# Optimization experiments

Hardware: AMD Instinct MI355X
Metric: run time of the kernel (lower is better)

Reference implementation:

```python
import jax, jax.numpy as jnp
import numpy as np

D_MODEL = 1024
NUM_HEADS = 16
D_HEAD = D_MODEL // NUM_HEADS


def setup_inputs() -> dict:
    key = jax.random.key(0)
    ks = jax.random.split(key, 7)
    B, S = 2, 2048
    scale = 1.0 / np.sqrt(D_MODEL)
    return {
        "x": jax.random.normal(ks[0], (B, S, D_MODEL), dtype=jnp.float32),
        "attn_weights": jnp.zeros((1,), dtype=jnp.float32),  # unused in original forward
        "Wq": jax.random.normal(ks[1], (D_MODEL, D_MODEL), dtype=jnp.float32) * scale,
        "Wk": jax.random.normal(ks[2], (D_MODEL, D_MODEL), dtype=jnp.float32) * scale,
        "Wv": jax.random.normal(ks[3], (D_MODEL, D_MODEL), dtype=jnp.float32) * scale,
        "Wp": jax.random.normal(ks[4], (D_MODEL, D_MODEL), dtype=jnp.float32) * scale,
        "bp": jnp.zeros((D_MODEL,), dtype=jnp.float32),
    }


def reference(x, attn_weights, Wq, Wk, Wv, Wp, bp):
    B, S, D = x.shape
    H, Dh = NUM_HEADS, D_HEAD
    # torch Linear: y = x @ W.T  (weights stored [out, in])
    q = (x @ Wq.T).reshape(B, S, H, Dh).transpose(0, 2, 1, 3)  # [B,H,S,Dh]
    k = (x @ Wk.T).reshape(B, S, H, Dh).transpose(0, 2, 1, 3)
    v = (x @ Wv.T).reshape(B, S, H, Dh).transpose(0, 2, 1, 3)
    # NOTE: original module applies NO 1/sqrt(d) scaling
    scores = jnp.einsum("bhqd,bhkd->bhqk", q, k)
    weights = jax.nn.softmax(scores, axis=-1)  # dropout is inference no-op
    out = jnp.einsum("bhqk,bhkd->bhqd", weights, v)
    out = out.transpose(0, 2, 1, 3).reshape(B, S, D)
    return out @ Wp.T + bp
```

## Files before the change

### kernel.cpp

```cpp
#include <hip/hip_runtime.h>
#include <hip/hip_bf16.h>

#define D_MODEL 1024
#define NUM_HEADS 16
#define D_HEAD 64
#define BATCH 2
#define SEQ 2048
#define TOKENS (BATCH * SEQ)

typedef __attribute__((ext_vector_type(8))) short bf16x8;
typedef __attribute__((ext_vector_type(4))) float f32x4;
typedef __attribute__((ext_vector_type(2))) unsigned int uint2v;

typedef __attribute__((address_space(1))) const unsigned int as1_uint;
typedef __attribute__((address_space(3))) unsigned int as3_uint;

#define LOG2E 1.44269504088896340736f

static __device__ __forceinline__ unsigned short f2bf(float f) {
    unsigned int u = __builtin_bit_cast(unsigned int, f);
    u += 0x7fffu + ((u >> 16) & 1u);
    return (unsigned short)(u >> 16);
}

static __device__ __forceinline__ unsigned int pk2bf(float a, float b) {
    __hip_bfloat162 h = __float22bfloat162_rn(float2{a, b});
    unsigned int u;
    __builtin_memcpy(&u, &h, 4);
    return u;
}

static __device__ __forceinline__ float fast_exp2(float x) {
    return __builtin_amdgcn_exp2f(x);
}

__global__ __launch_bounds__(256) void convert_bf16(
    const float* __restrict__ x,  const float* __restrict__ Wq,
    const float* __restrict__ Wk, const float* __restrict__ Wv,
    const float* __restrict__ Wp,
    unsigned short* __restrict__ xb,  unsigned short* __restrict__ Wqb,
    unsigned short* __restrict__ Wkb, unsigned short* __restrict__ Wvb,
    unsigned short* __restrict__ Wpb)
{
    int v = blockIdx.x * 256 + threadIdx.x;
    const float* s;
    unsigned short* d;
    int off;
    if (v < (1 << 20)) { s = x; d = xb; off = v; }
    else {
        int u = v - (1 << 20);
        int w = u >> 18;
        off = u & ((1 << 18) - 1);
        s = (w == 0) ? Wq : (w == 1) ? Wk : (w == 2) ? Wv : Wp;
        d = (w == 0) ? Wqb : (w == 1) ? Wkb : (w == 2) ? Wvb : Wpb;
    }
    float4 f = ((const float4*)s)[off];
    ushort4 o = { f2bf(f.x), f2bf(f.y), f2bf(f.z), f2bf(f.w) };
    ((ushort4*)d)[off] = o;
}

__global__ __launch_bounds__(512) void qkv_gemm(
    const unsigned short* __restrict__ xb,
    const unsigned short* __restrict__ Wqb, const unsigned short* __restrict__ Wkb,
    const unsigned short* __restrict__ Wvb,
    unsigned short* __restrict__ Q, unsigned short* __restrict__ Kb,
    unsigned short* __restrict__ Vt)
{
    const int m0 = blockIdx.x * 128;
    const int n0 = blockIdx.y * 128;
    const unsigned short* W = (blockIdx.z == 0) ? Wqb : (blockIdx.z == 1) ? Wkb : Wvb;

    __shared__ __attribute__((aligned(16))) unsigned short lA[128 * 64];
    __shared__ __attribute__((aligned(16))) unsigned short lB[128 * 64];

    const int t = threadIdx.x;
    const int wave = t >> 6, lane = t & 63;
    const int wm = (wave & 1) * 64, wn = (wave >> 1) * 32;
    const int l15 = lane & 15, quad = lane >> 4;
    const int sw = l15 & 7;

    f32x4 acc[4][2];
#pragma unroll
    for (int i = 0; i < 4; i++)
#pragma unroll
        for (int j = 0; j < 2; j++) acc[i][j] = (f32x4)0.f;

    for (int k0 = 0; k0 < D_MODEL; k0 += 64) {
        __syncthreads();
#pragma unroll
        for (int i = 0; i < 2; i++) {
            int fbase = wave * 64 + i * 512;
            int f = fbase + lane;
            int row = f >> 3, cp = f & 7;
            int c = cp ^ (row & 7);
            __builtin_amdgcn_global_load_lds(
                (as1_uint*)&xb[(size_t)(m0 + row) * D_MODEL + k0 + c * 8],
                (as3_uint*)&lA[fbase * 8], 16, 0, 0);
            __builtin_amdgcn_global_load_lds(
                (as1_uint*)&W[(size_t)(n0 + row) * D_MODEL + k0 + c * 8],
                (as3_uint*)&lB[fbase * 8], 16, 0, 0);
        }
        __syncthreads();

#pragma unroll
        for (int kk = 0; kk < 2; kk++) {
            const int cc = ((kk * 4 + quad) ^ sw) * 8;
            bf16x8 a[4], b[2];
#pragma unroll
            for (int mt = 0; mt < 4; mt++)
                a[mt] = *(const bf16x8*)&lA[(wm + mt * 16 + l15) * 64 + cc];
#pragma unroll
            for (int nt = 0; nt < 2; nt++)
                b[nt] = *(const bf16x8*)&lB[(wn + nt * 16 + l15) * 64 + cc];
#pragma unroll
            for (int mt = 0; mt < 4; mt++)
#pragma unroll
                for (int nt = 0; nt < 2; nt++)
                    acc[mt][nt] = __builtin_amdgcn_mfma_f32_16x16x32_bf16(
                        a[mt], b[nt], acc[mt][nt], 0, 0, 0);
        }
    }

    if (blockIdx.z == 2) {
        const int b = m0 >> 11;
        const int srow = (m0 & 2047) + wm + quad * 4;
#pragma unroll
        for (int mt = 0; mt < 4; mt++)
#pragma unroll
            for (int nt = 0; nt < 2; nt++) {
                int col = n0 + wn + nt * 16 + l15;
                int h = col >> 6, dh = col & 63;
                ushort4 pk = { f2bf(acc[mt][nt][0]), f2bf(acc[mt][nt][1]),
                               f2bf(acc[mt][nt][2]), f2bf(acc[mt][nt][3]) };
                *(ushort4*)&Vt[(size_t)((b * 16 + h) * 64 + dh) * SEQ + srow + mt * 16] = pk;
            }
    } else {
        unsigned short* Yo = (blockIdx.z == 0) ? Q : Kb;
        const float sc = (blockIdx.z == 0) ? LOG2E : 1.0f;
#pragma unroll
        for (int mt = 0; mt < 4; mt++)
#pragma unroll
            for (int nt = 0; nt < 2; nt++)
#pragma unroll
                for (int r = 0; r < 4; r++) {
                    int row = m0 + wm + mt * 16 + quad * 4 + r;
                    int col = n0 + wn + nt * 16 + l15;
                    Yo[(size_t)row * D_MODEL + col] = f2bf(acc[mt][nt][r] * sc);
                }
    }
}

__global__ __launch_bounds__(512, 4) void attn(
    const unsigned short* __restrict__ Q, const unsigned short* __restrict__ K,
    const unsigned short* __restrict__ Vt, unsigned short* __restrict__ O)
{
    const int q0 = blockIdx.x * 128;
    const int bh = blockIdx.y;
    const int b = bh >> 4, h = bh & 15;
    const size_t base = (size_t)b * SEQ * D_MODEL + (size_t)h * D_HEAD;
    const size_t baseV = (size_t)bh * D_HEAD * SEQ;

    __shared__ __attribute__((aligned(16))) char smem[40960];
    unsigned short* lK0 = (unsigned short*)&smem[0];
    unsigned short* lV0 = (unsigned short*)&smem[16384];

    const int t = threadIdx.x;
    const int wave = t >> 6, lane = t & 63;
    const int l15 = lane & 15, quad = lane >> 4;
    const int wq = wave & 3;
    const int sh = wave >> 2;
    const int qw = q0 + wq * 32;
    const int sbase = sh * (SEQ / 2);

    unsigned short* lK  = lK0 + sh * 4096;
    unsigned short* lVt = lV0 + sh * 4096;

    bf16x8 ones;
#pragma unroll
    for (int i = 0; i < 8; i++) ones[i] = (short)0x3F80;

    bf16x8 bq[2][2];
#pragma unroll
    for (int mq = 0; mq < 2; mq++)
#pragma unroll
        for (int kk = 0; kk < 2; kk++)
            bq[mq][kk] = *(const bf16x8*)&Q[base +
                (size_t)(qw + mq * 16 + l15) * D_MODEL + kk * 32 + quad * 8];

    const int tl = t & 255;
    const int r0 = tl >> 3, c0 = tl & 7;
    const int cs = (c0 ^ (r0 & 7)) * 8;
    const unsigned short* gK0 = &K[base + (size_t)(sbase + r0) * D_MODEL + c0 * 8];
    const unsigned short* gK1 = &K[base + (size_t)(sbase + r0 + 32) * D_MODEL + c0 * 8];
    const unsigned short* gV0 = &Vt[baseV + (size_t)r0 * SEQ + sbase + c0 * 8];
    const unsigned short* gV1 = &Vt[baseV + (size_t)(r0 + 32) * SEQ + sbase + c0 * 8];

    const int sw = l15 & 7;

    f32x4 o_acc[2][4];
#pragma unroll
    for (int i = 0; i < 2; i++)
#pragma unroll
        for (int j = 0; j < 4; j++) o_acc[i][j] = (f32x4)0.f;
    f32x4 o_l[2];
#pragma unroll
    for (int i = 0; i < 2; i++) o_l[i] = (f32x4)0.f;

    uint4 rK0 = *(const uint4*)gK0;
    uint4 rK1 = *(const uint4*)gK1;
    uint4 rV0 = *(const uint4*)gV0;
    uint4 rV1 = *(const uint4*)gV1;

    for (int s0 = 0; s0 < SEQ / 2; s0 += 64) {
        __syncthreads();
        *(uint4*)&lK[r0 * 64 + cs]        = rK0;
        *(uint4*)&lK[(r0 + 32) * 64 + cs] = rK1;
        *(uint4*)&lVt[r0 * 64 + cs]        = rV0;
        *(uint4*)&lVt[(r0 + 32) * 64 + cs] = rV1;
        __syncthreads();

        int sn = (s0 + 64 < SEQ / 2) ? s0 + 64 : 0;
        rK0 = *(const uint4*)(gK0 + (size_t)sn * D_MODEL);
        rK1 = *(const uint4*)(gK1 + (size_t)sn * D_MODEL);
        rV0 = *(const uint4*)(gV0 + sn);
        rV1 = *(const uint4*)(gV1 + sn);

        f32x4 st[4][2];
#pragma unroll
        for (int mt = 0; mt < 4; mt++)
#pragma unroll
            for (int mq = 0; mq < 2; mq++) st[mt][mq] = (f32x4)0.f;
#pragma unroll
        for (int kk = 0; kk < 2; kk++) {
            const int cc = ((kk * 4 + quad) ^ sw) * 8;
#pragma unroll
            for (int mt = 0; mt < 4; mt++) {
                bf16x8 ak = *(const bf16x8*)&lK[(mt * 16 + l15) * 64 + cc];
#pragma unroll
                for (int mq = 0; mq < 2; mq++)
                    st[mt][mq] = __builtin_amdgcn_mfma_f32_16x16x32_bf16(
                        ak, bq[mq][kk], st[mt][mq], 0, 0, 0);
            }
        }

#pragma unroll
        for (int mq = 0; mq < 2; mq++)
#pragma unroll
            for (int mt = 0; mt < 4; mt++)
#pragma unroll
                for (int r = 0; r < 4; r++)
                    st[mt][mq][r] = fast_exp2(st[mt][mq][r]);

        bf16x8 pa[2][2];
#pragma unroll
        for (int mq = 0; mq < 2; mq++)
#pragma unroll
            for (int kk = 0; kk < 2; kk++) {
                unsigned int cw[4];
#pragma unroll
                for (int j = 0; j < 2; j++) {
                    unsigned int w0 = pk2bf(st[2 * kk][mq][2 * j],
                                            st[2 * kk][mq][2 * j + 1]);
                    unsigned int w1 = pk2bf(st[2 * kk + 1][mq][2 * j],
                                            st[2 * kk + 1][mq][2 * j + 1]);
                    uint2v uv = __builtin_amdgcn_permlane32_swap(w0, w1, false, false);
                    uint2v f  = __builtin_amdgcn_permlane16_swap(uv[0], uv[1], false, false);
                    cw[j]     = f[0];
                    cw[2 + j] = f[1];
                }
                union { unsigned int w[4]; bf16x8 v; } u;
                u.w[0] = cw[0]; u.w[1] = cw[1]; u.w[2] = cw[2]; u.w[3] = cw[3];
                pa[mq][kk] = u.v;
            }

#pragma unroll
        for (int kk = 0; kk < 2; kk++) {
            const int cc = ((kk * 4 + quad) ^ sw) * 8;
            bf16x8 bv[4];
#pragma unroll
            for (int nt = 0; nt < 4; nt++)
                bv[nt] = *(const bf16x8*)&lVt[(nt * 16 + l15) * 64 + cc];
#pragma unroll
            for (int mq = 0; mq < 2; mq++) {
#pragma unroll
                for (int nt = 0; nt < 4; nt++)
                    o_acc[mq][nt] = __builtin_amdgcn_mfma_f32_16x16x32_bf16(
                        pa[mq][kk], bv[nt], o_acc[mq][nt], 0, 0, 0);
                o_l[mq] = __builtin_amdgcn_mfma_f32_16x16x32_bf16(
                    pa[mq][kk], ones, o_l[mq], 0, 0, 0);
            }
        }
    }

    float* sO = (float*)&smem[0];
    float* sL = (float*)&smem[36864];
    __syncthreads();
    if (sh == 1) {
#pragma unroll
        for (int mq = 0; mq < 2; mq++) {
#pragma unroll
            for (int r = 0; r < 4; r++)
                sL[wq * 32 + mq * 16 + quad * 4 + r] = o_l[mq][r];
#pragma unroll
            for (int nt = 0; nt < 4; nt++)
#pragma unroll
                for (int r = 0; r < 4; r++)
                    sO[(wq * 32 + mq * 16 + quad * 4 + r) * 68 + nt * 16 + l15] =
                        o_acc[mq][nt][r];
        }
    }
    __syncthreads();
    if (sh == 0) {
#pragma unroll
        for (int mq = 0; mq < 2; mq++) {
            float inv[4];
#pragma unroll
            for (int r = 0; r < 4; r++)
                inv[r] = 1.f / (o_l[mq][r] + sL[wq * 32 + mq * 16 + quad * 4 + r]);
#pragma unroll
            for (int nt = 0; nt < 4; nt++)
#pragma unroll
                for (int r = 0; r < 4; r++) {
                    int row = qw + mq * 16 + quad * 4 + r;
                    float v = o_acc[mq][nt][r] +
                              sO[(wq * 32 + mq * 16 + quad * 4 + r) * 68 + nt * 16 + l15];
                    O[base + (size_t)row * D_MODEL + nt * 16 + l15] = f2bf(v * inv[r]);
                }
        }
    }
}

__global__ __launch_bounds__(512) void proj_gemm(
    const unsigned short* __restrict__ A, const unsigned short* __restrict__ W,
    const float* __restrict__ bias, float* __restrict__ out)
{
    const int m0 = blockIdx.x * 128;
    const int n0 = blockIdx.y * 128;

    __shared__ __attribute__((aligned(16))) unsigned short lA[128 * 64];
    __shared__ __attribute__((aligned(16))) unsigned short lB[128 * 64];

    const int t = threadIdx.x;
    const int wave = t >> 6, lane = t & 63;
    const int wm = (wave & 1) * 64, wn = (wave >> 1) * 32;
    const int l15 = lane & 15, quad = lane >> 4;
    const int sw = l15 & 7;

    f32x4 acc[4][2];
#pragma unroll
    for (int i = 0; i < 4; i++)
#pragma unroll
        for (int j = 0; j < 2; j++) acc[i][j] = (f32x4)0.f;

    for (int k0 = 0; k0 < D_MODEL; k0 += 64) {
        __syncthreads();
#pragma unroll
        for (int i = 0; i < 2; i++) {
            int fbase = wave * 64 + i * 512;
            int f = fbase + lane;
            int row = f >> 3, cp = f & 7;
            int c = cp ^ (row & 7);
            __builtin_amdgcn_global_load_lds(
                (as1_uint*)&A[(size_t)(m0 + row) * D_MODEL + k0 + c * 8],
                (as3_uint*)&lA[fbase * 8], 16, 0, 0);
            __builtin_amdgcn_global_load_lds(
                (as1_uint*)&W[(size_t)(n0 + row) * D_MODEL + k0 + c * 8],
                (as3_uint*)&lB[fbase * 8], 16, 0, 0);
        }
        __syncthreads();

#pragma unroll
        for (int kk = 0; kk < 2; kk++) {
            const int cc = ((kk * 4 + quad) ^ sw) * 8;
            bf16x8 a[4], b[2];
#pragma unroll
            for (int mt = 0; mt < 4; mt++)
                a[mt] = *(const bf16x8*)&lA[(wm + mt * 16 + l15) * 64 + cc];
#pragma unroll
            for (int nt = 0; nt < 2; nt++)
                b[nt] = *(const bf16x8*)&lB[(wn + nt * 16 + l15) * 64 + cc];
#pragma unroll
            for (int mt = 0; mt < 4; mt++)
#pragma unroll
                for (int nt = 0; nt < 2; nt++)
                    acc[mt][nt] = __builtin_amdgcn_mfma_f32_16x16x32_bf16(
                        a[mt], b[nt], acc[mt][nt], 0, 0, 0);
        }
    }

#pragma unroll
    for (int mt = 0; mt < 4; mt++)
#pragma unroll
        for (int nt = 0; nt < 2; nt++)
#pragma unroll
            for (int r = 0; r < 4; r++) {
                int row = m0 + wm + mt * 16 + quad * 4 + r;
                int col = n0 + wn + nt * 16 + l15;
                out[(size_t)row * D_MODEL + col] = acc[mt][nt][r] + bias[col];
            }
}

extern "C" void kernel_launch(void* const* d_in, const int* in_sizes, int n_in,
                              void* d_out, int out_size, void* d_ws, size_t ws_size,
                              hipStream_t stream)
{
    const float* x  = (const float*)d_in[0];
    const float* Wq = (const float*)d_in[2];
    const float* Wk = (const float*)d_in[3];
    const float* Wv = (const float*)d_in[4];
    const float* Wp = (const float*)d_in[5];
    const float* bp = (const float*)d_in[6];
    float* out = (float*)d_out;

    unsigned short* Q   = (unsigned short*)d_ws;
    unsigned short* K   = Q   + (size_t)TOKENS * D_MODEL;
    unsigned short* Vt  = K   + (size_t)TOKENS * D_MODEL;
    unsigned short* O   = Vt  + (size_t)TOKENS * D_MODEL;
    unsigned short* xb  = O   + (size_t)TOKENS * D_MODEL;
    unsigned short* Wqb = xb  + (size_t)TOKENS * D_MODEL;
    unsigned short* Wkb = Wqb + (size_t)D_MODEL * D_MODEL;
    unsigned short* Wvb = Wkb + (size_t)D_MODEL * D_MODEL;
    unsigned short* Wpb = Wvb + (size_t)D_MODEL * D_MODEL;

    convert_bf16<<<8192, 256, 0, stream>>>(x, Wq, Wk, Wv, Wp,
                                           xb, Wqb, Wkb, Wvb, Wpb);
    qkv_gemm<<<dim3(TOKENS / 128, D_MODEL / 128, 3), 512, 0, stream>>>(
        xb, Wqb, Wkb, Wvb, Q, K, Vt);
    attn<<<dim3(SEQ / 128, BATCH * NUM_HEADS), 512, 0, stream>>>(Q, K, Vt, O);
    proj_gemm<<<dim3(TOKENS / 128, D_MODEL / 128), 512, 0, stream>>>(O, Wpb, bp, out);
}
```

Measured before the change: 188.2 us.

## Double-buffer K/V tiles in LDS and raise wave priority around MFMA blocks

The attention kernel now keeps two LDS buffers for the K and V^T tiles. Each iteration writes the next tile into the alternate buffer and computes on the current one, which drops one of the two __syncthreads per iteration. Global prefetch runs two tiles ahead. s_setprio raises wave priority around the MFMA sections to help interleave compute with other waves. LDS use grows from 40KB to 64KB, which can cut the number of resident 512-thread blocks per CU (launch bounds ask for 4).

Measured after the change: 185.7 us. No clear change (-1.3%).

```diff
diff --git a/kernel.cpp b/kernel.cpp
--- a/kernel.cpp
+++ b/kernel.cpp
@@ -160,9 +160,7 @@
     const size_t base = (size_t)b * SEQ * D_MODEL + (size_t)h * D_HEAD;
     const size_t baseV = (size_t)bh * D_HEAD * SEQ;
 
-    __shared__ __attribute__((aligned(16))) char smem[40960];
-    unsigned short* lK0 = (unsigned short*)&smem[0];
-    unsigned short* lV0 = (unsigned short*)&smem[16384];
+    __shared__ __attribute__((aligned(16))) char smem[65536];
 
     const int t = threadIdx.x;
     const int wave = t >> 6, lane = t & 63;
@@ -172,8 +170,8 @@
     const int qw = q0 + wq * 32;
     const int sbase = sh * (SEQ / 2);
 
-    unsigned short* lK  = lK0 + sh * 4096;
-    unsigned short* lVt = lV0 + sh * 4096;
+    unsigned short* lKb = (unsigned short*)&smem[sh * 8192];
+    unsigned short* lVb = (unsigned short*)&smem[32768 + sh * 8192];
 
     bf16x8 ones;
 #pragma unroll
@@ -210,38 +208,55 @@
     uint4 rK1 = *(const uint4*)gK1;
     uint4 rV0 = *(const uint4*)gV0;
     uint4 rV1 = *(const uint4*)gV1;
-
+    *(uint4*)&lKb[r0 * 64 + cs]        = rK0;
+    *(uint4*)&lKb[(r0 + 32) * 64 + cs] = rK1;
+    *(uint4*)&lVb[r0 * 64 + cs]        = rV0;
+    *(uint4*)&lVb[(r0 + 32) * 64 + cs] = rV1;
+    rK0 = *(const uint4*)(gK0 + (size_t)64 * D_MODEL);
+    rK1 = *(const uint4*)(gK1 + (size_t)64 * D_MODEL);
+    rV0 = *(const uint4*)(gV0 + 64);
+    rV1 = *(const uint4*)(gV1 + 64);
+
+    int cur = 0;
     for (int s0 = 0; s0 < SEQ / 2; s0 += 64) {
         __syncthreads();
-        *(uint4*)&lK[r0 * 64 + cs]        = rK0;
-        *(uint4*)&lK[(r0 + 32) * 64 + cs] = rK1;
-        *(uint4*)&lVt[r0 * 64 + cs]        = rV0;
-        *(uint4*)&lVt[(r0 + 32) * 64 + cs] = rV1;
-        __syncthreads();
-
-        int sn = (s0 + 64 < SEQ / 2) ? s0 + 64 : 0;
-        rK0 = *(const uint4*)(gK0 + (size_t)sn * D_MODEL);
-        rK1 = *(const uint4*)(gK1 + (size_t)sn * D_MODEL);
-        rV0 = *(const uint4*)(gV0 + sn);
-        rV1 = *(const uint4*)(gV1 + sn);
+        if (s0 + 64 < SEQ / 2) {
+            unsigned short* lKw = lKb + (cur ^ 1) * 8192;
+            unsigned short* lVw = lVb + (cur ^ 1) * 8192;
+            *(uint4*)&lKw[r0 * 64 + cs]        = rK0;
+            *(uint4*)&lKw[(r0 + 32) * 64 + cs] = rK1;
+            *(uint4*)&lVw[r0 * 64 + cs]        = rV0;
+            *(uint4*)&lVw[(r0 + 32) * 64 + cs] = rV1;
+        }
+        if (s0 + 128 < SEQ / 2) {
+            int sn = s0 + 128;
+            rK0 = *(const uint4*)(gK0 + (size_t)sn * D_MODEL);
+            rK1 = *(const uint4*)(gK1 + (size_t)sn * D_MODEL);
+            rV0 = *(const uint4*)(gV0 + sn);
+            rV1 = *(const uint4*)(gV1 + sn);
+        }
+        const unsigned short* lKc = lKb + cur * 8192;
+        const unsigned short* lVc = lVb + cur * 8192;
 
         f32x4 st[4][2];
 #pragma unroll
         for (int mt = 0; mt < 4; mt++)
 #pragma unroll
             for (int mq = 0; mq < 2; mq++) st[mt][mq] = (f32x4)0.f;
+        __builtin_amdgcn_s_setprio(1);
 #pragma unroll
         for (int kk = 0; kk < 2; kk++) {
             const int cc = ((kk * 4 + quad) ^ sw) * 8;
 #pragma unroll
             for (int mt = 0; mt < 4; mt++) {
-                bf16x8 ak = *(const bf16x8*)&lK[(mt * 16 + l15) * 64 + cc];
+                bf16x8 ak = *(const bf16x8*)&lKc[(mt * 16 + l15) * 64 + cc];
 #pragma unroll
                 for (int mq = 0; mq < 2; mq++)
                     st[mt][mq] = __builtin_amdgcn_mfma_f32_16x16x32_bf16(
                         ak, bq[mq][kk], st[mt][mq], 0, 0, 0);
             }
         }
+        __builtin_amdgcn_s_setprio(0);
 
 #pragma unroll
         for (int mq = 0; mq < 2; mq++)
@@ -273,13 +288,14 @@
                 pa[mq][kk] = u.v;
             }
 
+        __builtin_amdgcn_s_setprio(1);
 #pragma unroll
         for (int kk = 0; kk < 2; kk++) {
             const int cc = ((kk * 4 + quad) ^ sw) * 8;
             bf16x8 bv[4];
 #pragma unroll
             for (int nt = 0; nt < 4; nt++)
-                bv[nt] = *(const bf16x8*)&lVt[(nt * 16 + l15) * 64 + cc];
+                bv[nt] = *(const bf16x8*)&lVc[(nt * 16 + l15) * 64 + cc];
 #pragma unroll
             for (int mq = 0; mq < 2; mq++) {
 #pragma unroll
@@ -290,6 +306,8 @@
                     pa[mq][kk], ones, o_l[mq], 0, 0, 0);
             }
         }
+        __builtin_amdgcn_s_setprio(0);
+        cur ^= 1;
     }
 
     float* sO = (float*)&smem[0];
```

## Fuse Q/K/V projections into one block sharing the x tile, with double-buffered LDS

Applied to the files above, without the earlier changes.

The QKV GEMM now computes all three projections in a single block, so each x tile loaded into LDS is reused across Wq, Wk and Wv instead of being reloaded by three separate blocks. Global-to-LDS loads are double-buffered, with the next k-slice staged while the current one is multiplied, and the grid drops its z dimension. This cuts redundant x traffic and hides load latency. In exchange the block uses 128KB of LDS and three times the accumulator registers, which lowers occupancy, and the grid shrinks to 256 blocks.

New measurement: 179.9 us. 1.05x faster.

```diff
diff --git a/kernel.cpp b/kernel.cpp
--- a/kernel.cpp
+++ b/kernel.cpp
@@ -68,10 +68,8 @@
 {
     const int m0 = blockIdx.x * 128;
     const int n0 = blockIdx.y * 128;
-    const unsigned short* W = (blockIdx.z == 0) ? Wqb : (blockIdx.z == 1) ? Wkb : Wvb;
-
-    __shared__ __attribute__((aligned(16))) unsigned short lA[128 * 64];
-    __shared__ __attribute__((aligned(16))) unsigned short lB[128 * 64];
+
+    __shared__ __attribute__((aligned(16))) unsigned short sm[65536];
 
     const int t = threadIdx.x;
     const int wave = t >> 6, lane = t & 63;
@@ -79,49 +77,82 @@
     const int l15 = lane & 15, quad = lane >> 4;
     const int sw = l15 & 7;
 
-    f32x4 acc[4][2];
-#pragma unroll
-    for (int i = 0; i < 4; i++)
-#pragma unroll
-        for (int j = 0; j < 2; j++) acc[i][j] = (f32x4)0.f;
-
-    for (int k0 = 0; k0 < D_MODEL; k0 += 64) {
-        __syncthreads();
+    const unsigned short* Wz[3] = { Wqb, Wkb, Wvb };
+
+    f32x4 acc[3][4][2];
+#pragma unroll
+    for (int z = 0; z < 3; z++)
+#pragma unroll
+        for (int i = 0; i < 4; i++)
+#pragma unroll
+            for (int j = 0; j < 2; j++) acc[z][i][j] = (f32x4)0.f;
+
+    auto stage = [&](int k0, int buf) {
 #pragma unroll
         for (int i = 0; i < 2; i++) {
             int fbase = wave * 64 + i * 512;
             int f = fbase + lane;
             int row = f >> 3, cp = f & 7;
             int c = cp ^ (row & 7);
+            int srcc = k0 + c * 8;
             __builtin_amdgcn_global_load_lds(
-                (as1_uint*)&xb[(size_t)(m0 + row) * D_MODEL + k0 + c * 8],
-                (as3_uint*)&lA[fbase * 8], 16, 0, 0);
-            __builtin_amdgcn_global_load_lds(
-                (as1_uint*)&W[(size_t)(n0 + row) * D_MODEL + k0 + c * 8],
-                (as3_uint*)&lB[fbase * 8], 16, 0, 0);
-        }
-        __syncthreads();
-
+                (as1_uint*)&xb[(size_t)(m0 + row) * D_MODEL + srcc],
+                (as3_uint*)&sm[buf * 32768 + fbase * 8], 16, 0, 0);
+#pragma unroll
+            for (int z = 0; z < 3; z++)
+                __builtin_amdgcn_global_load_lds(
+                    (as1_uint*)&Wz[z][(size_t)(n0 + row) * D_MODEL + srcc],
+                    (as3_uint*)&sm[buf * 32768 + (1 + z) * 8192 + fbase * 8],
+                    16, 0, 0);
+        }
+    };
+
+    stage(0, 0);
+    __syncthreads();
+
+    int cur = 0;
+    for (int k0 = 0; k0 < D_MODEL; k0 += 64) {
+        if (k0 + 64 < D_MODEL) stage(k0 + 64, cur ^ 1);
+
+        const unsigned short* lA = &sm[cur * 32768];
 #pragma unroll
         for (int kk = 0; kk < 2; kk++) {
             const int cc = ((kk * 4 + quad) ^ sw) * 8;
-            bf16x8 a[4], b[2];
+            bf16x8 a[4];
 #pragma unroll
             for (int mt = 0; mt < 4; mt++)
                 a[mt] = *(const bf16x8*)&lA[(wm + mt * 16 + l15) * 64 + cc];
 #pragma unroll
-            for (int nt = 0; nt < 2; nt++)
-                b[nt] = *(const bf16x8*)&lB[(wn + nt * 16 + l15) * 64 + cc];
-#pragma unroll
-            for (int mt = 0; mt < 4; mt++)
+            for (int z = 0; z < 3; z++) {
+                const unsigned short* lB = &sm[cur * 32768 + (1 + z) * 8192];
+                bf16x8 b[2];
 #pragma unroll
                 for (int nt = 0; nt < 2; nt++)
-                    acc[mt][nt] = __builtin_amdgcn_mfma_f32_16x16x32_bf16(
-                        a[mt], b[nt], acc[mt][nt], 0, 0, 0);
-        }
-    }
-
-    if (blockIdx.z == 2) {
+                    b[nt] = *(const bf16x8*)&lB[(wn + nt * 16 + l15) * 64 + cc];
+#pragma unroll
+                for (int mt = 0; mt < 4; mt++)
+#pragma unroll
+                    for (int nt = 0; nt < 2; nt++)
+                        acc[z][mt][nt] = __builtin_amdgcn_mfma_f32_16x16x32_bf16(
+                            a[mt], b[nt], acc[z][mt][nt], 0, 0, 0);
+            }
+        }
+        __syncthreads();
+        cur ^= 1;
+    }
+
+#pragma unroll
+    for (int mt = 0; mt < 4; mt++)
+#pragma unroll
+        for (int nt = 0; nt < 2; nt++)
+#pragma unroll
+            for (int r = 0; r < 4; r++) {
+                int row = m0 + wm + mt * 16 + quad * 4 + r;
+                int col = n0 + wn + nt * 16 + l15;
+                Q[(size_t)row * D_MODEL + col]  = f2bf(acc[0][mt][nt][r] * LOG2E);
+                Kb[(size_t)row * D_MODEL + col] = f2bf(acc[1][mt][nt][r]);
+            }
+    {
         const int b = m0 >> 11;
         const int srow = (m0 & 2047) + wm + quad * 4;
 #pragma unroll
@@ -130,23 +161,10 @@
             for (int nt = 0; nt < 2; nt++) {
                 int col = n0 + wn + nt * 16 + l15;
                 int h = col >> 6, dh = col & 63;
-                ushort4 pk = { f2bf(acc[mt][nt][0]), f2bf(acc[mt][nt][1]),
-                               f2bf(acc[mt][nt][2]), f2bf(acc[mt][nt][3]) };
+                ushort4 pk = { f2bf(acc[2][mt][nt][0]), f2bf(acc[2][mt][nt][1]),
+                               f2bf(acc[2][mt][nt][2]), f2bf(acc[2][mt][nt][3]) };
                 *(ushort4*)&Vt[(size_t)((b * 16 + h) * 64 + dh) * SEQ + srow + mt * 16] = pk;
             }
-    } else {
-        unsigned short* Yo = (blockIdx.z == 0) ? Q : Kb;
-        const float sc = (blockIdx.z == 0) ? LOG2E : 1.0f;
-#pragma unroll
-        for (int mt = 0; mt < 4; mt++)
-#pragma unroll
-            for (int nt = 0; nt < 2; nt++)
-#pragma unroll
-                for (int r = 0; r < 4; r++) {
-                    int row = m0 + wm + mt * 16 + quad * 4 + r;
-                    int col = n0 + wn + nt * 16 + l15;
-                    Yo[(size_t)row * D_MODEL + col] = f2bf(acc[mt][nt][r] * sc);
-                }
     }
 }
 
@@ -424,7 +442,7 @@
 
     convert_bf16<<<8192, 256, 0, stream>>>(x, Wq, Wk, Wv, Wp,
                                            xb, Wqb, Wkb, Wvb, Wpb);
-    qkv_gemm<<<dim3(TOKENS / 128, D_MODEL / 128, 3), 512, 0, stream>>>(
+    qkv_gemm<<<dim3(TOKENS / 128, D_MODEL / 128), 512, 0, stream>>>(
         xb, Wqb, Wkb, Wvb, Q, K, Vt);
     attn<<<dim3(SEQ / 128, BATCH * NUM_HEADS), 512, 0, stream>>>(Q, K, Vt, O);
     proj_gemm<<<dim3(TOKENS / 128, D_MODEL / 128), 512, 0, stream>>>(O, Wpb, bp, out);
```
